# Kernel tuning notes

Measured on AMD Instinct MI355X. Metric: run time of the kernel, lower is better.

## Reference

```python
import jax, jax.numpy as jnp
import numpy as np

M = 8192      # nodes
D = 128       # feature dim
DEG = 32      # neighbors per node


def setup_inputs() -> dict:
    key = jax.random.key(0)
    ks = jax.random.split(key, 6)
    z = jax.random.normal(ks[0], (M, D), dtype=jnp.float32)
    # deterministic, duplicate-free edge list: node i -> (i+1..i+DEG) mod M
    src = jnp.repeat(jnp.arange(M, dtype=jnp.int64), DEG)
    dst = (src + jnp.tile(jnp.arange(1, DEG + 1, dtype=jnp.int64), M)) % M
    edge_index = jnp.stack([src, dst], axis=0)  # [2, M*DEG]
    s = 1.0 / np.sqrt(D)
    Wg = jax.random.normal(ks[1], (D, D), dtype=jnp.float32) * s
    Wc = jax.random.normal(ks[2], (D, D), dtype=jnp.float32) * s
    Wq = jax.random.normal(ks[3], (D, D), dtype=jnp.float32) * s
    Wk = jax.random.normal(ks[4], (D, D), dtype=jnp.float32) * s
    a = jax.random.normal(ks[5], (2 * D,), dtype=jnp.float32)
    return {"z": z, "edge_index": edge_index, "Wg": Wg, "Wc": Wc,
            "Wq": Wq, "Wk": Wk, "a": a}


def reference(z, edge_index, Wg, Wc, Wq, Wk, a):
    m, d = z.shape
    wg = z @ Wg.T                              # [m, d]
    src, dst = edge_index[0], edge_index[1]
    a_src, a_dst = a[:d], a[d:]
    # per-edge score: leaky_relu(a . [wg[i], wg[j]]) = leaky_relu(a1.wg[i] + a2.wg[j])
    scores = jax.nn.leaky_relu((wg @ a_src)[src] + (wg @ a_dst)[dst])  # [E]
    # softmax over each source node's neighbors (segment softmax)
    smax = jax.ops.segment_max(scores, src, num_segments=m)
    ex = jnp.exp(scores - smax[src])
    denom = jax.ops.segment_sum(ex, src, num_segments=m)
    alpha = ex / denom[src]                    # [E]
    # scatter-aggregate: local[i] = sum_j alpha_ij * wg[j]
    local = jax.ops.segment_sum(alpha[:, None] * wg[dst], src, num_segments=m)
    # dense global attention branch
    q = z @ Wq.T
    k = z @ Wk.T
    beta = jax.nn.softmax(q @ k.T / jnp.sqrt(jnp.float32(d)), axis=-1)  # [m, m]
    global_msg = beta @ (z @ Wc.T)
    return jax.nn.leaky_relu(local + global_msg + z)
```

## Files before the change

### kernel.cpp

```cpp
#include <hip/hip_runtime.h>

#define MM 8192
#define DD 128
#define DEG 32
#define KSPLIT 16
#define BK 32
#define NTILE 16
#define NB 16
#define RSTAGE 48

typedef __attribute__((ext_vector_type(8))) _Float16 h8;
typedef __attribute__((ext_vector_type(4))) float f4;
typedef __attribute__((ext_vector_type(4))) unsigned int u4;
typedef __attribute__((ext_vector_type(4))) short s4;

__device__ __forceinline__ unsigned short f2h(float f) {
  _Float16 h = (_Float16)f;
  return __builtin_bit_cast(unsigned short, h);
}

__device__ __forceinline__ void lds_dma16(const unsigned short* gptr, unsigned short* lptr) {
  __builtin_amdgcn_global_load_lds(
      (const __attribute__((address_space(1))) unsigned int*)gptr,
      (__attribute__((address_space(3))) unsigned int*)lptr, 16, 0, 0);
}

__global__ __launch_bounds__(256) void proj_kernel(
    const float* __restrict__ z, const float* __restrict__ Wg,
    const float* __restrict__ Wc, const float* __restrict__ Wq,
    const float* __restrict__ Wk, const float* __restrict__ a,
    float* __restrict__ wg, unsigned short* __restrict__ qb,
    unsigned short* __restrict__ kb, unsigned short* __restrict__ ct,
    float* __restrict__ sg, float* __restrict__ sd)
{
  __shared__ unsigned short zt[64 * 136];
  __shared__ unsigned short wt[128 * 136];
  const int mode = blockIdx.y;
  const float* __restrict__ W = (mode == 0) ? Wg : (mode == 1) ? Wq : (mode == 2) ? Wk : Wc;
  const int r0 = blockIdx.x * 64;
  const int tid = threadIdx.x;

  #pragma unroll
  for (int it = 0; it < 8; ++it) {
    int id = tid + it * 256, row = id >> 5, c4 = (id & 31) * 4;
    f4 v = *(const f4*)(z + (r0 + row) * DD + c4);
    s4 sv = {(short)f2h(v.x), (short)f2h(v.y), (short)f2h(v.z), (short)f2h(v.w)};
    *(s4*)&zt[row * 136 + c4] = sv;
  }
  #pragma unroll
  for (int it = 0; it < 16; ++it) {
    int id = tid + it * 256, row = id >> 5, c4 = (id & 31) * 4;
    f4 v = *(const f4*)(W + row * DD + c4);
    s4 sv = {(short)f2h(v.x), (short)f2h(v.y), (short)f2h(v.z), (short)f2h(v.w)};
    *(s4*)&wt[row * 136 + c4] = sv;
  }
  __syncthreads();

  const int lane = tid & 63, w = tid >> 6, n = lane & 15, quad = lane >> 4;
  h8 afr[4];
  #pragma unroll
  for (int kt = 0; kt < 4; ++kt)
    afr[kt] = *(const h8*)&zt[(16 * w + n) * 136 + kt * 32 + quad * 8];

  f4 acc[8];
  const f4 fzero = {0.f, 0.f, 0.f, 0.f};
  #pragma unroll
  for (int nt = 0; nt < 8; ++nt) {
    f4 c = fzero;
    #pragma unroll
    for (int kt = 0; kt < 4; ++kt) {
      h8 b = *(const h8*)&wt[(16 * nt + n) * 136 + kt * 32 + quad * 8];
      c = __builtin_amdgcn_mfma_f32_16x16x32_f16(afr[kt], b, c, 0, 0, 0);
    }
    acc[nt] = c;
  }

  if (mode == 0) {
    #pragma unroll
    for (int nt = 0; nt < 8; ++nt)
      #pragma unroll
      for (int r = 0; r < 4; ++r)
        wg[(r0 + 16 * w + quad * 4 + r) * DD + 16 * nt + n] = acc[nt][r];
    float av[8], bv[8];
    #pragma unroll
    for (int nt = 0; nt < 8; ++nt) { av[nt] = a[16 * nt + n]; bv[nt] = a[DD + 16 * nt + n]; }
    #pragma unroll
    for (int r = 0; r < 4; ++r) {
      float s1 = 0.f, s2 = 0.f;
      #pragma unroll
      for (int nt = 0; nt < 8; ++nt) { s1 += acc[nt][r] * av[nt]; s2 += acc[nt][r] * bv[nt]; }
      s1 += __shfl_xor(s1, 1); s1 += __shfl_xor(s1, 2); s1 += __shfl_xor(s1, 4); s1 += __shfl_xor(s1, 8);
      s2 += __shfl_xor(s2, 1); s2 += __shfl_xor(s2, 2); s2 += __shfl_xor(s2, 4); s2 += __shfl_xor(s2, 8);
      if (n == 0) {
        int g = r0 + 16 * w + quad * 4 + r;
        sg[g] = s1; sd[g] = s2;
      }
    }
  } else if (mode == 1) {
    const float qscale = 0.12752551286084110f;
    #pragma unroll
    for (int nt = 0; nt < 8; ++nt)
      #pragma unroll
      for (int r = 0; r < 4; ++r)
        qb[(r0 + 16 * w + quad * 4 + r) * DD + 16 * nt + n] = f2h(acc[nt][r] * qscale);
  } else if (mode == 2) {
    #pragma unroll
    for (int nt = 0; nt < 8; ++nt)
      #pragma unroll
      for (int r = 0; r < 4; ++r)
        kb[(r0 + 16 * w + quad * 4 + r) * DD + 16 * nt + n] = f2h(acc[nt][r]);
  } else {
    __syncthreads();
    #pragma unroll
    for (int nt = 0; nt < 8; ++nt)
      #pragma unroll
      for (int r = 0; r < 4; ++r)
        wt[(16 * nt + n) * 80 + 16 * w + quad * 4 + r] = f2h(acc[nt][r]);
    __syncthreads();
    #pragma unroll
    for (int it = 0; it < 4; ++it) {
      int idx = tid + it * 256, d = idx >> 3, c8 = (idx & 7) * 8;
      u4 v = *(const u4*)&wt[d * 80 + c8];
      *(u4*)(ct + (size_t)d * MM + r0 + c8) = v;
    }
  }
}

__global__ __launch_bounds__(256, 2) void flash_kernel(
    const unsigned short* __restrict__ qb, const unsigned short* __restrict__ kb,
    const unsigned short* __restrict__ ct, unsigned short* __restrict__ Opart,
    float* __restrict__ Lpart)
{
  __shared__ unsigned short sh[18944];
  const int bid = blockIdx.x + (blockIdx.y << 6);
  const int ck = bid & 15, qt = bid >> 4;
  const int tid = threadIdx.x, lane = tid & 63, w = tid >> 6;
  const int n = lane & 15, quad = lane >> 4;
  const int qr0 = qt * 128;

  #pragma unroll
  for (int it = 0; it < 8; ++it)
    lds_dma16(qb + (qr0 + it * 16 + n) * DD + w * 32 + quad * 8,
              &sh[(it * 256 + tid) * 8]);
  __syncthreads();
  h8 aq[2][4];
  #pragma unroll
  for (int mt = 0; mt < 2; ++mt)
    #pragma unroll
    for (int kt = 0; kt < 4; ++kt)
      aq[mt][kt] = *(const h8*)&sh[((w * 2 + mt) * 4 + kt) * 512 + lane * 8];
  __syncthreads();

  const unsigned short* kp = kb + (size_t)(ck * 512 + 2 * n) * DD + w * 32 + quad * 8;
  const unsigned short* vp = ct + (size_t)(16 * w + n) * MM + ck * 512 + quad * 8;

  #pragma unroll
  for (int it = 0; it < 2; ++it)
    lds_dma16(kp + it * DD, &sh[(it * 256 + tid) * 8]);

  f4 acc_o[2][8];
  f4 accs[2][2];
  h8 ap[2];
  const f4 fzero = {0.f, 0.f, 0.f, 0.f};
  #pragma unroll
  for (int mt = 0; mt < 2; ++mt)
    #pragma unroll
    for (int dt = 0; dt < 8; ++dt) acc_o[mt][dt] = fzero;
  float l_r[2][4] = {{0.f, 0.f, 0.f, 0.f}, {0.f, 0.f, 0.f, 0.f}};
  const int pbase = 16384 + w * 640;

#define QK_TILE(CUR)                                                          \
  { accs[0][0] = fzero; accs[0][1] = fzero;                                   \
    accs[1][0] = fzero; accs[1][1] = fzero;                                   \
    __builtin_amdgcn_s_setprio(1);                                            \
    _Pragma("unroll")                                                         \
    for (int nt = 0; nt < 2; ++nt) {                                          \
      _Pragma("unroll")                                                       \
      for (int kt = 0; kt < 4; ++kt) {                                        \
        h8 bk = *(const h8*)&sh[(CUR) + nt * 2048 + kt * 512 + lane * 8];     \
        accs[0][nt] = __builtin_amdgcn_mfma_f32_16x16x32_f16(aq[0][kt], bk, accs[0][nt], 0, 0, 0); \
        accs[1][nt] = __builtin_amdgcn_mfma_f32_16x16x32_f16(aq[1][kt], bk, accs[1][nt], 0, 0, 0); \
      }                                                                       \
    }                                                                         \
    __builtin_amdgcn_s_setprio(0); }

#define PV_TILE(PRV)                                                          \
  { __builtin_amdgcn_s_setprio(1);                                            \
    _Pragma("unroll")                                                         \
    for (int dt = 0; dt < 8; ++dt) {                                          \
      h8 bv = *(const h8*)&sh[(PRV) + 4096 + dt * 512 + lane * 8];            \
      acc_o[0][dt] = __builtin_amdgcn_mfma_f32_16x16x32_f16(ap[0], bv, acc_o[0][dt], 0, 0, 0); \
      acc_o[1][dt] = __builtin_amdgcn_mfma_f32_16x16x32_f16(ap[1], bv, acc_o[1][dt], 0, 0, 0); \
    }                                                                         \
    __builtin_amdgcn_s_setprio(0); }

#define SOFTMAX_TILE                                                          \
  { _Pragma("unroll")                                                         \
    for (int mt = 0; mt < 2; ++mt) {                                          \
      _Pragma("unroll")                                                       \
      for (int r = 0; r < 4; ++r) {                                           \
        float p0 = exp2f(fminf(accs[mt][0][r], 14.4269504f));                 \
        float p1 = exp2f(fminf(accs[mt][1][r], 14.4269504f));                 \
        l_r[mt][r] += p0 + p1;                                                \
        auto pv2 = __builtin_amdgcn_cvt_pkrtz(p0, p1);      \
        *(unsigned int*)&sh[pbase + (quad * 4 + r) * 40 + 2 * n] =            \
            __builtin_bit_cast(unsigned int, pv2);                            \
      }                                                                       \
      ap[mt] = *(const h8*)&sh[pbase + n * 40 + quad * 8];                    \
    }                                                                         \
  }

  __syncthreads();
  #pragma unroll
  for (int it = 0; it < 2; ++it)
    lds_dma16(kp + BK * DD + it * DD, &sh[8192 + (it * 256 + tid) * 8]);
  #pragma unroll
  for (int it = 0; it < 2; ++it)
    lds_dma16(vp + (size_t)it * 64 * MM, &sh[4096 + (it * 256 + tid) * 8]);
  QK_TILE(0)
  SOFTMAX_TILE

  for (int t = 1; t < NTILE; ++t) {
    __syncthreads();
    const int cur = (t & 1) * 8192;
    const int prv = cur ^ 8192;

    if (t < NTILE - 1) {
      const unsigned short* kpn = kp + (size_t)(t + 1) * BK * DD;
      #pragma unroll
      for (int it = 0; it < 2; ++it)
        lds_dma16(kpn + it * DD, &sh[prv + (it * 256 + tid) * 8]);
    }
    {
      const unsigned short* vpn = vp + t * BK;
      #pragma unroll
      for (int it = 0; it < 2; ++it)
        lds_dma16(vpn + (size_t)it * 64 * MM, &sh[cur + 4096 + (it * 256 + tid) * 8]);
    }

    QK_TILE(cur)
    PV_TILE(prv)
    SOFTMAX_TILE
  }

  __syncthreads();
  PV_TILE(8192)

  #pragma unroll
  for (int mt = 0; mt < 2; ++mt)
    #pragma unroll
    for (int r = 0; r < 4; ++r) {
      float lv = l_r[mt][r];
      lv += __shfl_xor(lv, 1); lv += __shfl_xor(lv, 2);
      lv += __shfl_xor(lv, 4); lv += __shfl_xor(lv, 8);
      int g = qr0 + w * 32 + mt * 16 + quad * 4 + r;
      if (n == 0) Lpart[ck * MM + g] = lv;
      #pragma unroll
      for (int dt = 0; dt < 8; ++dt)
        Opart[((size_t)ck * MM + g) * DD + 16 * dt + n] = f2h(acc_o[mt][dt][r]);
    }
#undef QK_TILE
#undef PV_TILE
#undef SOFTMAX_TILE
}

__global__ __launch_bounds__(256) void merge_kernel(
    const int* __restrict__ ei, const float* __restrict__ wg,
    const float* __restrict__ sg, const float* __restrict__ sd,
    const unsigned short* __restrict__ Opart, const float* __restrict__ Lpart,
    const float* __restrict__ z, float* __restrict__ out)
{
  __shared__ float rows_s[RSTAGE * 132];
  __shared__ float sc_s[NB][DEG];
  __shared__ float alpha_s[NB][DEG];
  __shared__ int idx_s[NB][DEG];
  const int tid = threadIdx.x;
  const int i0 = blockIdx.x * NB;

  #pragma unroll
  for (int it = 0; it < 6; ++it) {
    int idx = tid + it * 256;
    int r = idx >> 5, c4 = (idx & 31) * 4;
    int grow = (i0 + 1 + r) & (MM - 1);
    *(f4*)&rows_s[r * 132 + c4] = *(const f4*)(wg + (size_t)grow * DD + c4);
  }
  #pragma unroll
  for (int it = 0; it < 2; ++it) {
    int e = tid + it * 256;
    int nj = e >> 5, j = e & 31;
    int i = i0 + nj;
    int dstj = ei[MM * DEG + i * DEG + j];
    float s = sg[i] + sd[dstj];
    sc_s[nj][j] = s > 0.f ? s : 0.01f * s;
    idx_s[nj][j] = (dstj - (i0 + 1)) & (MM - 1);
  }
  __syncthreads();

  const int ni = tid >> 4, l16 = tid & 15;
  {
    float s0 = sc_s[ni][l16], s1 = sc_s[ni][l16 + 16];
    float mx = fmaxf(s0, s1);
    mx = fmaxf(mx, __shfl_xor(mx, 1)); mx = fmaxf(mx, __shfl_xor(mx, 2));
    mx = fmaxf(mx, __shfl_xor(mx, 4)); mx = fmaxf(mx, __shfl_xor(mx, 8));
    float p0 = __expf(s0 - mx), p1 = __expf(s1 - mx);
    float sum = p0 + p1;
    sum += __shfl_xor(sum, 1); sum += __shfl_xor(sum, 2);
    sum += __shfl_xor(sum, 4); sum += __shfl_xor(sum, 8);
    float inv = 1.f / sum;
    alpha_s[ni][l16] = p0 * inv;
    alpha_s[ni][l16 + 16] = p1 * inv;
  }

  const int d0 = l16 * 8;
  const int i = i0 + ni;
  float acc[8] = {0.f, 0.f, 0.f, 0.f, 0.f, 0.f, 0.f, 0.f};
  #pragma unroll 4
  for (int j = 0; j < DEG; ++j) {
    float al = alpha_s[ni][j];
    int r = idx_s[ni][j];
    if (r < RSTAGE) {
      const float* src = &rows_s[r * 132 + d0];
      #pragma unroll
      for (int q = 0; q < 8; ++q) acc[q] += al * src[q];
    } else {
      const float* src = wg + (size_t)((i0 + 1 + r) & (MM - 1)) * DD + d0;
      #pragma unroll
      for (int q = 0; q < 8; ++q) acc[q] += al * src[q];
    }
  }

  float l = 0.f;
  float o[8] = {0.f, 0.f, 0.f, 0.f, 0.f, 0.f, 0.f, 0.f};
  #pragma unroll
  for (int ck = 0; ck < KSPLIT; ++ck) {
    l += Lpart[ck * MM + i];
    h8 v = *(const h8*)(Opart + ((size_t)ck * MM + i) * DD + d0);
    #pragma unroll
    for (int q = 0; q < 8; ++q) o[q] += (float)v[q];
  }
  float inv = 1.0f / l;
  const float* zp = z + (size_t)i * DD + d0;
  float* op = out + (size_t)i * DD + d0;
  #pragma unroll
  for (int q = 0; q < 8; ++q) {
    float r = o[q] * inv + acc[q] + zp[q];
    op[q] = r > 0.f ? r : 0.01f * r;
  }
}

extern "C" void kernel_launch(void* const* d_in, const int* in_sizes, int n_in,
                              void* d_out, int out_size, void* d_ws, size_t ws_size,
                              hipStream_t stream) {
  const float* z  = (const float*)d_in[0];
  const int*   ei = (const int*)d_in[1];
  const float* Wg = (const float*)d_in[2];
  const float* Wc = (const float*)d_in[3];
  const float* Wq = (const float*)d_in[4];
  const float* Wk = (const float*)d_in[5];
  const float* a  = (const float*)d_in[6];
  float* out = (float*)d_out;
  char* ws = (char*)d_ws;

  float*          wg    = (float*)(ws + 0);
  unsigned short* qb    = (unsigned short*)(ws + (4 << 20));
  unsigned short* kb    = (unsigned short*)(ws + (6 << 20));
  unsigned short* ct    = (unsigned short*)(ws + (8 << 20));
  float*          sg    = (float*)(ws + (10 << 20));
  float*          sd    = (float*)(ws + (10 << 20) + (64 << 10));
  unsigned short* Opart = (unsigned short*)(ws + (11 << 20));
  float*          Lpart = (float*)(ws + (43 << 20));

  proj_kernel<<<dim3(128, 4), 256, 0, stream>>>(z, Wg, Wc, Wq, Wk, a, wg, qb, kb, ct, sg, sd);
  flash_kernel<<<dim3(64, KSPLIT), 256, 0, stream>>>(qb, kb, ct, Opart, Lpart);
  merge_kernel<<<512, 256, 0, stream>>>(ei, wg, sg, sd, Opart, Lpart, z, out);
}
```

Before: 133.7 us.

## Double flash key tile to 64 and halve key-split count to 8

Each flash block now processes 64 keys per iteration instead of 32 and covers twice as many keys, so the key dimension is split 8 ways instead of 16. The QK, softmax and PV macros, the LDS layout, the DMA staging and the P-matrix layout are widened to match, and the Lpart workspace offset moves because the Opart buffer is halved. The aim is to cut per-tile synchronisation overhead and halve the partial-output traffic the merge kernel has to read. In exchange each block needs about twice the LDS and more registers, and there are half as many blocks to spread across the CUs.

```diff
diff --git a/kernel.cpp b/kernel.cpp
--- a/kernel.cpp
+++ b/kernel.cpp
@@ -3,8 +3,8 @@
 #define MM 8192
 #define DD 128
 #define DEG 32
-#define KSPLIT 16
-#define BK 32
+#define KSPLIT 8
+#define BK 64
 #define NTILE 16
 #define NB 16
 #define RSTAGE 48
@@ -131,9 +131,9 @@
     const unsigned short* __restrict__ ct, unsigned short* __restrict__ Opart,
     float* __restrict__ Lpart)
 {
-  __shared__ unsigned short sh[18944];
+  __shared__ unsigned short sh[37376];
   const int bid = blockIdx.x + (blockIdx.y << 6);
-  const int ck = bid & 15, qt = bid >> 4;
+  const int ck = bid & 7, qt = bid >> 3;
   const int tid = threadIdx.x, lane = tid & 63, w = tid >> 6;
   const int n = lane & 15, quad = lane >> 4;
   const int qr0 = qt * 128;
@@ -151,30 +151,30 @@
       aq[mt][kt] = *(const h8*)&sh[((w * 2 + mt) * 4 + kt) * 512 + lane * 8];
   __syncthreads();
 
-  const unsigned short* kp = kb + (size_t)(ck * 512 + 2 * n) * DD + w * 32 + quad * 8;
-  const unsigned short* vp = ct + (size_t)(16 * w + n) * MM + ck * 512 + quad * 8;
-
-  #pragma unroll
-  for (int it = 0; it < 2; ++it)
+  const unsigned short* kp = kb + (size_t)(ck * 1024 + 4 * n) * DD + w * 32 + quad * 8;
+  const unsigned short* vp = ct + (size_t)(16 * (w >> 1) + n) * MM + ck * 1024 + (w & 1) * 32 + quad * 8;
+
+  #pragma unroll
+  for (int it = 0; it < 4; ++it)
     lds_dma16(kp + it * DD, &sh[(it * 256 + tid) * 8]);
 
   f4 acc_o[2][8];
-  f4 accs[2][2];
-  h8 ap[2];
+  f4 accs[2][4];
+  h8 ap[2][2];
   const f4 fzero = {0.f, 0.f, 0.f, 0.f};
   #pragma unroll
   for (int mt = 0; mt < 2; ++mt)
     #pragma unroll
     for (int dt = 0; dt < 8; ++dt) acc_o[mt][dt] = fzero;
   float l_r[2][4] = {{0.f, 0.f, 0.f, 0.f}, {0.f, 0.f, 0.f, 0.f}};
-  const int pbase = 16384 + w * 640;
+  const int pbase = 32768 + w * 1152;
 
 #define QK_TILE(CUR)                                                          \
-  { accs[0][0] = fzero; accs[0][1] = fzero;                                   \
-    accs[1][0] = fzero; accs[1][1] = fzero;                                   \
+  { accs[0][0] = fzero; accs[0][1] = fzero; accs[0][2] = fzero; accs[0][3] = fzero; \
+    accs[1][0] = fzero; accs[1][1] = fzero; accs[1][2] = fzero; accs[1][3] = fzero; \
     __builtin_amdgcn_s_setprio(1);                                            \
     _Pragma("unroll")                                                         \
-    for (int nt = 0; nt < 2; ++nt) {                                          \
+    for (int nt = 0; nt < 4; ++nt) {                                          \
       _Pragma("unroll")                                                       \
       for (int kt = 0; kt < 4; ++kt) {                                        \
         h8 bk = *(const h8*)&sh[(CUR) + nt * 2048 + kt * 512 + lane * 8];     \
@@ -188,9 +188,12 @@
   { __builtin_amdgcn_s_setprio(1);                                            \
     _Pragma("unroll")                                                         \
     for (int dt = 0; dt < 8; ++dt) {                                          \
-      h8 bv = *(const h8*)&sh[(PRV) + 4096 + dt * 512 + lane * 8];            \
-      acc_o[0][dt] = __builtin_amdgcn_mfma_f32_16x16x32_f16(ap[0], bv, acc_o[0][dt], 0, 0, 0); \
-      acc_o[1][dt] = __builtin_amdgcn_mfma_f32_16x16x32_f16(ap[1], bv, acc_o[1][dt], 0, 0, 0); \
+      _Pragma("unroll")                                                       \
+      for (int k2 = 0; k2 < 2; ++k2) {                                        \
+        h8 bv = *(const h8*)&sh[(PRV) + 8192 + dt * 1024 + k2 * 512 + lane * 8]; \
+        acc_o[0][dt] = __builtin_amdgcn_mfma_f32_16x16x32_f16(ap[0][k2], bv, acc_o[0][dt], 0, 0, 0); \
+        acc_o[1][dt] = __builtin_amdgcn_mfma_f32_16x16x32_f16(ap[1][k2], bv, acc_o[1][dt], 0, 0, 0); \
+      }                                                                       \
     }                                                                         \
     __builtin_amdgcn_s_setprio(0); }
 
@@ -201,41 +204,46 @@
       for (int r = 0; r < 4; ++r) {                                           \
         float p0 = exp2f(fminf(accs[mt][0][r], 14.4269504f));                 \
         float p1 = exp2f(fminf(accs[mt][1][r], 14.4269504f));                 \
-        l_r[mt][r] += p0 + p1;                                                \
-        auto pv2 = __builtin_amdgcn_cvt_pkrtz(p0, p1);      \
-        *(unsigned int*)&sh[pbase + (quad * 4 + r) * 40 + 2 * n] =            \
-            __builtin_bit_cast(unsigned int, pv2);                            \
+        float p2 = exp2f(fminf(accs[mt][2][r], 14.4269504f));                 \
+        float p3 = exp2f(fminf(accs[mt][3][r], 14.4269504f));                 \
+        l_r[mt][r] += (p0 + p1) + (p2 + p3);                                  \
+        auto pk0 = __builtin_amdgcn_cvt_pkrtz(p0, p1);                        \
+        auto pk1 = __builtin_amdgcn_cvt_pkrtz(p2, p3);                        \
+        uint2 pv2; pv2.x = __builtin_bit_cast(unsigned int, pk0);             \
+        pv2.y = __builtin_bit_cast(unsigned int, pk1);                        \
+        *(uint2*)&sh[pbase + (quad * 4 + r) * 72 + n * 4] = pv2;              \
       }                                                                       \
-      ap[mt] = *(const h8*)&sh[pbase + n * 40 + quad * 8];                    \
+      ap[mt][0] = *(const h8*)&sh[pbase + n * 72 + quad * 8];                 \
+      ap[mt][1] = *(const h8*)&sh[pbase + n * 72 + 32 + quad * 8];            \
     }                                                                         \
   }
 
   __syncthreads();
   #pragma unroll
-  for (int it = 0; it < 2; ++it)
-    lds_dma16(kp + BK * DD + it * DD, &sh[8192 + (it * 256 + tid) * 8]);
-  #pragma unroll
-  for (int it = 0; it < 2; ++it)
-    lds_dma16(vp + (size_t)it * 64 * MM, &sh[4096 + (it * 256 + tid) * 8]);
+  for (int it = 0; it < 4; ++it)
+    lds_dma16(kp + BK * DD + it * DD, &sh[16384 + (it * 256 + tid) * 8]);
+  #pragma unroll
+  for (int it = 0; it < 4; ++it)
+    lds_dma16(vp + (size_t)it * 32 * MM, &sh[8192 + (it * 256 + tid) * 8]);
   QK_TILE(0)
   SOFTMAX_TILE
 
   for (int t = 1; t < NTILE; ++t) {
     __syncthreads();
-    const int cur = (t & 1) * 8192;
-    const int prv = cur ^ 8192;
+    const int cur = (t & 1) * 16384;
+    const int prv = cur ^ 16384;
 
     if (t < NTILE - 1) {
       const unsigned short* kpn = kp + (size_t)(t + 1) * BK * DD;
       #pragma unroll
-      for (int it = 0; it < 2; ++it)
+      for (int it = 0; it < 4; ++it)
         lds_dma16(kpn + it * DD, &sh[prv + (it * 256 + tid) * 8]);
     }
     {
       const unsigned short* vpn = vp + t * BK;
       #pragma unroll
-      for (int it = 0; it < 2; ++it)
-        lds_dma16(vpn + (size_t)it * 64 * MM, &sh[cur + 4096 + (it * 256 + tid) * 8]);
+      for (int it = 0; it < 4; ++it)
+        lds_dma16(vpn + (size_t)it * 32 * MM, &sh[cur + 8192 + (it * 256 + tid) * 8]);
     }
 
     QK_TILE(cur)
@@ -244,7 +252,7 @@
   }
 
   __syncthreads();
-  PV_TILE(8192)
+  PV_TILE(16384)
 
   #pragma unroll
   for (int mt = 0; mt < 2; ++mt)
@@ -368,7 +376,7 @@
   float*          sg    = (float*)(ws + (10 << 20));
   float*          sd    = (float*)(ws + (10 << 20) + (64 << 10));
   unsigned short* Opart = (unsigned short*)(ws + (11 << 20));
-  float*          Lpart = (float*)(ws + (43 << 20));
+  float*          Lpart = (float*)(ws + (27 << 20));
 
   proj_kernel<<<dim3(128, 4), 256, 0, stream>>>(z, Wg, Wc, Wq, Wk, a, wg, qb, kb, ct, sg, sd);
   flash_kernel<<<dim3(64, KSPLIT), 256, 0, stream>>>(qb, kb, ct, Opart, Lpart);
```

After: 126.4 us. 1.06x faster.
